# Kernel optimization log

Measured on AMD Instinct MI355X. Metric: run time of the kernel, lower is better.

The kernel has to match this reference:

```python
import jax, jax.numpy as jnp
import numpy as np

THETA = 5.0  # cache sharpness (init arg `theta`)
D_FEAT = 2048
N_MEM = 200000
N_CLASSES = 1000


def setup_inputs() -> dict:
    key = jax.random.key(0)
    k1, k2, k3 = jax.random.split(key, 3)
    x = jax.random.normal(k1, (1, D_FEAT), dtype=jnp.float32)  # backbone output
    mem_keys = jax.random.normal(k2, (D_FEAT, N_MEM), dtype=jnp.float32)
    mem_vals = jax.random.uniform(k3, (N_MEM, N_CLASSES), dtype=jnp.float32)
    return {"x": x, "mem_keys": mem_keys, "mem_vals": mem_vals}


def reference(x, mem_keys, mem_vals):
    # squeeze -> [D]; global L2 normalize (torch.norm over whole tensor)
    v = jnp.squeeze(x)
    v = v / jnp.linalg.norm(v)
    # single-query unnormalized attention over the memory bank
    similarities = jnp.exp(THETA * (v @ mem_keys))   # [N_MEM]
    p_mem = similarities @ mem_vals                  # [N_CLASSES]
    return jnp.log(p_mem).reshape(1, N_CLASSES)
```

## Files before the change

### kernel.cpp

```cpp
#include <hip/hip_runtime.h>
#include <math.h>

#define D_FEAT    2048
#define N_MEM     200000
#define N_CLASSES 1000
#define NC4       (N_CLASSES / 4)
#define THETA     5.0f
#define BLK       256
#define GRID      768
#define NQ_TOT    (N_MEM / 4)
#define QBASE     (NQ_TOT / GRID)
#define QREM      (NQ_TOT - QBASE * GRID)
#define DCHUNK    (D_FEAT / 4)
#define NM4       (N_MEM / 4)
#define MAXQ      (QBASE + 1)

__global__ __launch_bounds__(BLK) void cache_fused_kernel(
    const float* __restrict__ x,
    const float* __restrict__ K,
    const float* __restrict__ V,
    float*       __restrict__ acc)
{
    __shared__ float  x_lds[D_FEAT];
    __shared__ float4 partl[4][MAXQ];
    __shared__ float  sims[MAXQ * 4];
    __shared__ float  wred[BLK / 64];

    const int t = threadIdx.x;
    const int b = blockIdx.x;

    float ss = 0.f;
    const float4* x4 = (const float4*)x;
    #pragma unroll
    for (int k = 0; k < D_FEAT / 4 / BLK; ++k) {
        float4 v = x4[t + k * BLK];
        ((float4*)x_lds)[t + k * BLK] = v;
        ss += v.x * v.x + v.y * v.y + v.z * v.z + v.w * v.w;
    }
    #pragma unroll
    for (int off = 32; off >= 1; off >>= 1)
        ss += __shfl_xor(ss, off, 64);
    if ((t & 63) == 0) wred[t >> 6] = ss;
    __syncthreads();
    const float scale = THETA / sqrtf(wred[0] + wred[1] + wred[2] + wred[3]);

    const int qstart = QBASE * b + (b < QREM ? b : QREM);
    const int nq     = QBASE + (b < QREM ? 1 : 0);
    const int cstart = qstart * 4;
    const int ncols  = nq * 4;

    const int tx = t & 63;
    const int ty = t >> 6;
    const float* xp = x_lds + ty * DCHUNK;
    const float* kbase = K + (size_t)ty * DCHUNK * N_MEM;
    #pragma unroll
    for (int p = 0; p < 2; ++p) {
        const int qi = p * 64 + tx;
        if (qi < nq) {
            const int j = (qstart + qi) * 4;
            const float4* kp = (const float4*)(kbase + j);
            float4 a = make_float4(0.f, 0.f, 0.f, 0.f);
            #pragma unroll 8
            for (int dd = 0; dd < DCHUNK; ++dd) {
                const float  xv = xp[dd];
                const float4 kv = kp[(size_t)dd * NM4];
                a.x = fmaf(xv, kv.x, a.x);
                a.y = fmaf(xv, kv.y, a.y);
                a.z = fmaf(xv, kv.z, a.z);
                a.w = fmaf(xv, kv.w, a.w);
            }
            partl[ty][qi] = a;
        }
    }
    __syncthreads();

    if (t < nq) {
        const float4 s0 = partl[0][t], s1 = partl[1][t];
        const float4 s2 = partl[2][t], s3 = partl[3][t];
        sims[t * 4 + 0] = expf(scale * ((s0.x + s1.x) + (s2.x + s3.x)));
        sims[t * 4 + 1] = expf(scale * ((s0.y + s1.y) + (s2.y + s3.y)));
        sims[t * 4 + 2] = expf(scale * ((s0.z + s1.z) + (s2.z + s3.z)));
        sims[t * 4 + 3] = expf(scale * ((s0.w + s1.w) + (s2.w + s3.w)));
    }
    __syncthreads();

    if (t < NC4) {
        float4 a4 = make_float4(0.f, 0.f, 0.f, 0.f);
        const float4* Vp = (const float4*)V + (size_t)cstart * NC4 + t;
        for (int jj = 0; jj < ncols; ++jj) {
            const float  s  = sims[jj];
            const float4 vv = Vp[(size_t)jj * NC4];
            a4.x = fmaf(s, vv.x, a4.x);
            a4.y = fmaf(s, vv.y, a4.y);
            a4.z = fmaf(s, vv.z, a4.z);
            a4.w = fmaf(s, vv.w, a4.w);
        }
        atomicAdd(&acc[t * 4 + 0], a4.x);
        atomicAdd(&acc[t * 4 + 1], a4.y);
        atomicAdd(&acc[t * 4 + 2], a4.z);
        atomicAdd(&acc[t * 4 + 3], a4.w);
    }
}

__global__ void log_inplace_kernel(float* __restrict__ out)
{
    const int c = blockIdx.x * blockDim.x + threadIdx.x;
    if (c < N_CLASSES) out[c] = logf(out[c]);
}

extern "C" void kernel_launch(void* const* d_in, const int* in_sizes, int n_in,
                              void* d_out, int out_size, void* d_ws, size_t ws_size,
                              hipStream_t stream)
{
    const float* x = (const float*)d_in[0];
    const float* K = (const float*)d_in[1];
    const float* V = (const float*)d_in[2];
    float* out = (float*)d_out;

    hipMemsetAsync(out, 0, N_CLASSES * sizeof(float), stream);

    cache_fused_kernel<<<GRID, BLK, 0, stream>>>(x, K, V, out);
    log_inplace_kernel<<<(N_CLASSES + 255) / 256, 256, 0, stream>>>(out);
}
```

Baseline: 474.6 us.

## Align column partition to 32-column chunks and replace atomics with workspace reduction

Assigns each block whole groups of 32 memory columns, so K loads start on 128-byte boundaries. Per-block class partials go to a workspace and are summed in a dedicated reduce+log kernel instead of being added atomically after a memset. Loop unroll factors are also raised. In exchange, the coarser partition gives blocks less even work, and the workspace path needs about 3 MB of scratch space.

Result: faster. 417.5 us (-12.0%).

```diff
diff --git a/kernel.cpp b/kernel.cpp
--- a/kernel.cpp
+++ b/kernel.cpp
@@ -8,18 +8,19 @@
 #define THETA     5.0f
 #define BLK       256
 #define GRID      768
-#define NQ_TOT    (N_MEM / 4)
-#define QBASE     (NQ_TOT / GRID)
-#define QREM      (NQ_TOT - QBASE * GRID)
+#define OCT_TOT   (N_MEM / 32)
+#define OBASE     (OCT_TOT / GRID)
+#define OREM      (OCT_TOT - OBASE*GRID)
 #define DCHUNK    (D_FEAT / 4)
 #define NM4       (N_MEM / 4)
-#define MAXQ      (QBASE + 1)
+#define MAXQ      ((OBASE + 1) * 8)
 
+template<bool USE_WS>
 __global__ __launch_bounds__(BLK) void cache_fused_kernel(
     const float* __restrict__ x,
     const float* __restrict__ K,
     const float* __restrict__ V,
-    float*       __restrict__ acc)
+    float*       __restrict__ outp)
 {
     __shared__ float  x_lds[D_FEAT];
     __shared__ float4 partl[4][MAXQ];
@@ -44,23 +45,23 @@
     __syncthreads();
     const float scale = THETA / sqrtf(wred[0] + wred[1] + wred[2] + wred[3]);
 
-    const int qstart = QBASE * b + (b < QREM ? b : QREM);
-    const int nq     = QBASE + (b < QREM ? 1 : 0);
-    const int cstart = qstart * 4;
+    const int ostart = OBASE * b + (b < OREM ? b : OREM);
+    const int noct   = OBASE + (b < OREM ? 1 : 0);
+    const int qstart = ostart * 8;
+    const int nq     = noct * 8;
     const int ncols  = nq * 4;
 
     const int tx = t & 63;
     const int ty = t >> 6;
-    const float* xp = x_lds + ty * DCHUNK;
-    const float* kbase = K + (size_t)ty * DCHUNK * N_MEM;
+    const float*  xp = x_lds + ty * DCHUNK;
+    const float4* kb = (const float4*)K + (size_t)ty * DCHUNK * NM4 + qstart;
     #pragma unroll
     for (int p = 0; p < 2; ++p) {
         const int qi = p * 64 + tx;
         if (qi < nq) {
-            const int j = (qstart + qi) * 4;
-            const float4* kp = (const float4*)(kbase + j);
+            const float4* kp = kb + qi;
             float4 a = make_float4(0.f, 0.f, 0.f, 0.f);
-            #pragma unroll 8
+            #pragma unroll 16
             for (int dd = 0; dd < DCHUNK; ++dd) {
                 const float  xv = xp[dd];
                 const float4 kv = kp[(size_t)dd * NM4];
@@ -86,7 +87,8 @@
 
     if (t < NC4) {
         float4 a4 = make_float4(0.f, 0.f, 0.f, 0.f);
-        const float4* Vp = (const float4*)V + (size_t)cstart * NC4 + t;
+        const float4* Vp = (const float4*)V + (size_t)qstart * 4 * NC4 + t;
+        #pragma unroll 4
         for (int jj = 0; jj < ncols; ++jj) {
             const float  s  = sims[jj];
             const float4 vv = Vp[(size_t)jj * NC4];
@@ -95,10 +97,40 @@
             a4.z = fmaf(s, vv.z, a4.z);
             a4.w = fmaf(s, vv.w, a4.w);
         }
-        atomicAdd(&acc[t * 4 + 0], a4.x);
-        atomicAdd(&acc[t * 4 + 1], a4.y);
-        atomicAdd(&acc[t * 4 + 2], a4.z);
-        atomicAdd(&acc[t * 4 + 3], a4.w);
+        if (USE_WS) {
+            ((float4*)outp)[(size_t)b * NC4 + t] = a4;
+        } else {
+            atomicAdd(&outp[t * 4 + 0], a4.x);
+            atomicAdd(&outp[t * 4 + 1], a4.y);
+            atomicAdd(&outp[t * 4 + 2], a4.z);
+            atomicAdd(&outp[t * 4 + 3], a4.w);
+        }
+    }
+}
+
+__global__ __launch_bounds__(64) void reduce_log_kernel(
+    const float* __restrict__ ws, float* __restrict__ out)
+{
+    const int cq = blockIdx.x;
+    const int l  = threadIdx.x;
+    float4 s = make_float4(0.f, 0.f, 0.f, 0.f);
+    #pragma unroll
+    for (int b = l; b < GRID; b += 64) {
+        const float4 v = ((const float4*)ws)[(size_t)b * NC4 + cq];
+        s.x += v.x; s.y += v.y; s.z += v.z; s.w += v.w;
+    }
+    #pragma unroll
+    for (int off = 32; off >= 1; off >>= 1) {
+        s.x += __shfl_xor(s.x, off, 64);
+        s.y += __shfl_xor(s.y, off, 64);
+        s.z += __shfl_xor(s.z, off, 64);
+        s.w += __shfl_xor(s.w, off, 64);
+    }
+    if (l == 0) {
+        out[cq * 4 + 0] = logf(s.x);
+        out[cq * 4 + 1] = logf(s.y);
+        out[cq * 4 + 2] = logf(s.z);
+        out[cq * 4 + 3] = logf(s.w);
     }
 }
 
@@ -117,8 +149,14 @@
     const float* V = (const float*)d_in[2];
     float* out = (float*)d_out;
 
-    hipMemsetAsync(out, 0, N_CLASSES * sizeof(float), stream);
-
-    cache_fused_kernel<<<GRID, BLK, 0, stream>>>(x, K, V, out);
-    log_inplace_kernel<<<(N_CLASSES + 255) / 256, 256, 0, stream>>>(out);
+    const size_t ws_need = (size_t)GRID * N_CLASSES * sizeof(float);
+    if (ws_size >= ws_need) {
+        float* partials = (float*)d_ws;
+        cache_fused_kernel<true><<<GRID, BLK, 0, stream>>>(x, K, V, partials);
+        reduce_log_kernel<<<NC4, 64, 0, stream>>>(partials, out);
+    } else {
+        hipMemsetAsync(out, 0, N_CLASSES * sizeof(float), stream);
+        cache_fused_kernel<false><<<GRID, BLK, 0, stream>>>(x, K, V, out);
+        log_inplace_kernel<<<(N_CLASSES + 255) / 256, 256, 0, stream>>>(out);
+    }
 }
```
